# Optimization experiments

Hardware: AMD Instinct MI355X
Metric: run time of the kernel (lower is better)

## Reference

```python
import jax, jax.numpy as jnp
import numpy as np

N = 200000   # total nodes across batched graphs
E = 3200000  # total edges
G = 1024     # number of graphs
MOL_DIM, HID, OUT = 9, 64, 64


def gcn_conv(x, W, b, src, dst, num_nodes):
    """PyG GCNConv: add self-loops, symmetric deg^{-1/2} normalization, linear first."""
    x = x @ W  # [N, H]
    loop = jnp.arange(num_nodes, dtype=src.dtype)
    s = jnp.concatenate([src, loop])
    d = jnp.concatenate([dst, loop])
    deg = jax.ops.segment_sum(jnp.ones_like(d, dtype=x.dtype), d, num_segments=num_nodes)
    dinv = jnp.where(deg > 0, jax.lax.rsqrt(deg), 0.0)
    norm = dinv[s] * dinv[d]                       # [E+N]
    msgs = x[s] * norm[:, None]                    # gather + scale
    out = jax.ops.segment_sum(msgs, d, num_segments=num_nodes)  # scatter-add
    return out + b


def setup_inputs() -> dict:
    key = jax.random.key(0)
    ks = jax.random.split(key, 12)
    def glorot(k, shp):
        scale = np.sqrt(2.0 / (shp[0] + shp[1])).astype(np.float32)
        return jax.random.normal(k, shp, dtype=jnp.float32) * scale
    return {
        "x": jax.random.normal(ks[0], (N, MOL_DIM), dtype=jnp.float32),
        "edge_index": jax.random.randint(ks[1], (2, E), 0, N, dtype=jnp.int32),
        "edge_attr": jax.random.normal(ks[2], (E, 3), dtype=jnp.float32),
        "batch": jnp.sort(jax.random.randint(ks[3], (N,), 0, G, dtype=jnp.int32)),
        "W1": glorot(ks[4], (MOL_DIM, HID)), "b1": jnp.zeros((HID,), jnp.float32),
        "W2": glorot(ks[5], (HID, HID)),     "b2": jnp.zeros((HID,), jnp.float32),
        "W3": glorot(ks[6], (HID, HID)),     "b3": jnp.zeros((HID,), jnp.float32),
        "Wl": glorot(ks[7], (2 * HID, OUT)), "bl": jnp.zeros((OUT,), jnp.float32),
    }


def reference(x, edge_index, edge_attr, batch, W1, b1, W2, b2, W3, b3, Wl, bl):
    src, dst = edge_index[0], edge_index[1]
    h = jax.nn.relu(gcn_conv(x, W1, b1, src, dst, N))
    h = jax.nn.relu(gcn_conv(h, W2, b2, src, dst, N))
    h = jax.nn.relu(gcn_conv(h, W3, b3, src, dst, N))
    # global mean/max pool over graphs
    counts = jax.ops.segment_sum(jnp.ones((N,), h.dtype), batch, num_segments=G)
    h_sum = jax.ops.segment_sum(h, batch, num_segments=G)
    h_mean = h_sum / jnp.maximum(counts, 1.0)[:, None]
    h_max = jax.ops.segment_max(h, batch, num_segments=G)
    pooled = jnp.concatenate([h_mean, h_max], axis=1)   # [G, 2H]
    return pooled @ Wl + bl
```

## Files before the change

### kernel.cpp

```cpp
#include <hip/hip_runtime.h>

typedef unsigned short u16;
typedef __attribute__((ext_vector_type(8))) short short8;
typedef __attribute__((ext_vector_type(4))) float float4v;

#define HID 64
#define MOLD 9
#define BSH 10
#define NBM 256
#define NBLK 256

__device__ __forceinline__ float bf2f(u16 u) {
    return __uint_as_float(((unsigned)u) << 16);
}
__device__ __forceinline__ u16 f2bf(float f) {
    unsigned x = __float_as_uint(f);
    unsigned r = (x + 0x7FFFu + ((x >> 16) & 1u)) >> 16;
    return (u16)r;
}
__device__ __forceinline__ void unpack_add(uint4 r, float* a) {
    a[0] += __uint_as_float(r.x << 16); a[1] += __uint_as_float(r.x & 0xffff0000u);
    a[2] += __uint_as_float(r.y << 16); a[3] += __uint_as_float(r.y & 0xffff0000u);
    a[4] += __uint_as_float(r.z << 16); a[5] += __uint_as_float(r.z & 0xffff0000u);
    a[6] += __uint_as_float(r.w << 16); a[7] += __uint_as_float(r.w & 0xffff0000u);
}
__device__ __forceinline__ void unpack_set(uint4 r, float* a) {
    a[0] = __uint_as_float(r.x << 16); a[1] = __uint_as_float(r.x & 0xffff0000u);
    a[2] = __uint_as_float(r.y << 16); a[3] = __uint_as_float(r.y & 0xffff0000u);
    a[4] = __uint_as_float(r.z << 16); a[5] = __uint_as_float(r.z & 0xffff0000u);
    a[6] = __uint_as_float(r.w << 16); a[7] = __uint_as_float(r.w & 0xffff0000u);
}
__device__ __forceinline__ void unpack_add2(uint2 r, float* a) {
    a[0] += __uint_as_float(r.x << 16); a[1] += __uint_as_float(r.x & 0xffff0000u);
    a[2] += __uint_as_float(r.y << 16); a[3] += __uint_as_float(r.y & 0xffff0000u);
}

__global__ void k_detect(const u16* __restrict__ p, int n, int* __restrict__ flag) {
    bool bad = false;
    for (int i = threadIdx.x; i < n; i += 256) {
        float v = bf2f(p[i]);
        if (!(v == v) || fabsf(v) > 1000.f) bad = true;
    }
    if (bad) atomicOr(flag, 1);
}

__global__ void k_cvt_w(const void* W1, const void* b1, const void* W2, const void* b2,
                        const void* W3, const void* b3, const void* Wl, const void* bl,
                        const int* __restrict__ flag, u16* __restrict__ wbf) {
    int mode = *flag;
    int i = blockIdx.x * 256 + threadIdx.x;
    if (i >= 17216) return;
    const void* s; int base;
    if (i < 576)        { s = W1; base = 0; }
    else if (i < 640)   { s = b1; base = 576; }
    else if (i < 4736)  { s = W2; base = 640; }
    else if (i < 4800)  { s = b2; base = 4736; }
    else if (i < 8896)  { s = W3; base = 4800; }
    else if (i < 8960)  { s = b3; base = 8896; }
    else if (i < 17152) { s = Wl; base = 8960; }
    else                { s = bl; base = 17152; }
    int o = i - base;
    wbf[i] = mode ? f2bf(((const float*)s)[o]) : ((const u16*)s)[o];
}

__global__ __launch_bounds__(256) void k_hist(const int* __restrict__ ei, int E, int nb,
                                              int chunk, int* __restrict__ cntmat) {
    __shared__ int h[NBM];
    int tid = threadIdx.x, k = blockIdx.x;
    for (int i = tid; i < nb; i += 256) h[i] = 0;
    __syncthreads();
    int e0 = k * chunk, e1 = e0 + chunk; if (e1 > E) e1 = E;
    for (int e = e0 + tid; e < e1; e += 256)
        atomicAdd(&h[ei[E + e] >> BSH], 1);
    __syncthreads();
    for (int b = tid; b < nb; b += 256) cntmat[b * NBLK + k] = h[b];
}

__global__ __launch_bounds__(1024) void k_scanmat(int* __restrict__ cntmat, int total) {
    __shared__ int ps[1024];
    int tid = threadIdx.x;
    int chunk = (total + 1023) >> 10;
    int i0 = tid * chunk, i1 = i0 + chunk; if (i1 > total) i1 = total;
    int sum = 0;
    for (int i = i0; i < i1; i++) sum += cntmat[i];
    ps[tid] = sum;
    __syncthreads();
    for (int off = 1; off < 1024; off <<= 1) {
        int t = (tid >= off) ? ps[tid - off] : 0;
        __syncthreads();
        ps[tid] += t;
        __syncthreads();
    }
    int run = ps[tid] - sum;
    for (int i = i0; i < i1; i++) { int c = cntmat[i]; cntmat[i] = run; run += c; }
}

__global__ __launch_bounds__(256) void k_scatter(const int* __restrict__ ei, int E, int nb,
                                                 int chunk, const int* __restrict__ offmat,
                                                 unsigned* __restrict__ staging) {
    __shared__ int cur[NBM];
    int tid = threadIdx.x, k = blockIdx.x;
    for (int b = tid; b < nb; b += 256) cur[b] = offmat[b * NBLK + k];
    __syncthreads();
    int e0 = k * chunk, e1 = e0 + chunk; if (e1 > E) e1 = E;
    for (int e = e0 + tid; e < e1; e += 256) {
        int s = ei[e];
        int d = ei[E + e];
        int b = d >> BSH;
        int p = atomicAdd(&cur[b], 1);
        staging[p] = (unsigned)s | ((unsigned)(d & ((1 << BSH) - 1)) << 18);
    }
}

__global__ __launch_bounds__(256) void k_p4(const unsigned* __restrict__ staging,
                                            const int* __restrict__ offmat, int nb, int N, int E,
                                            int* __restrict__ col, int* __restrict__ rowptr,
                                            float* __restrict__ dinv) {
    __shared__ int cnt[1 << BSH];
    __shared__ int cur[1 << BSH];
    __shared__ int ps[256];
    int b = blockIdx.x, tid = threadIdx.x;
    int s0 = offmat[b * NBLK];
    int s1 = (b == nb - 1) ? E : offmat[(b + 1) * NBLK];
    for (int i = tid; i < (1 << BSH); i += 256) cnt[i] = 0;
    __syncthreads();
    for (int i = s0 + tid; i < s1; i += 256)
        atomicAdd(&cnt[staging[i] >> 18], 1);
    __syncthreads();
    int base4 = tid * 4;
    int c0 = cnt[base4], c1 = cnt[base4 + 1], c2 = cnt[base4 + 2], c3 = cnt[base4 + 3];
    int tsum = c0 + c1 + c2 + c3;
    ps[tid] = tsum;
    __syncthreads();
    for (int off = 1; off < 256; off <<= 1) {
        int t = (tid >= off) ? ps[tid - off] : 0;
        __syncthreads();
        ps[tid] += t;
        __syncthreads();
    }
    int ex = ps[tid] - tsum;
    int o0 = s0 + ex, o1 = o0 + c0, o2 = o1 + c1, o3 = o2 + c2;
    cur[base4] = o0; cur[base4 + 1] = o1; cur[base4 + 2] = o2; cur[base4 + 3] = o3;
    int v = (b << BSH) + base4;
    if (v < N)     { rowptr[v] = o0;     dinv[v] = rsqrtf((float)(c0 + 1)); }
    if (v + 1 < N) { rowptr[v + 1] = o1; dinv[v + 1] = rsqrtf((float)(c1 + 1)); }
    if (v + 2 < N) { rowptr[v + 2] = o2; dinv[v + 2] = rsqrtf((float)(c2 + 1)); }
    if (v + 3 < N) { rowptr[v + 3] = o3; dinv[v + 3] = rsqrtf((float)(c3 + 1)); }
    if (b == nb - 1 && tid == 0) rowptr[N] = E;
    __syncthreads();
    for (int i = s0 + tid; i < s1; i += 256) {
        unsigned w = staging[i];
        int p = atomicAdd(&cur[w >> 18], 1);
        col[p] = (int)(w & 0x3FFFF);
    }
}

__global__ void k_cvt_x(const void* __restrict__ x, const float* __restrict__ dinv,
                        const int* __restrict__ flag, int N, u16* __restrict__ xd) {
    int mode = *flag;
    int i = blockIdx.x * 256 + threadIdx.x;
    if (i >= N * 16) return;
    int v = i >> 4, f = i & 15;
    float val = 0.f;
    if (f < MOLD) {
        val = mode ? ((const float*)x)[v * MOLD + f]
                   : bf2f(((const u16*)x)[v * MOLD + f]);
        val *= dinv[v];
    }
    xd[i] = f2bf(val);
}

__global__ __launch_bounds__(256, 4) void k_aggx(
        const u16* __restrict__ xd, const int* __restrict__ rowptr,
        const int* __restrict__ col, const float* __restrict__ dinv,
        const u16* __restrict__ W1, const u16* __restrict__ b1,
        int N, u16* __restrict__ h1) {
    int lane = threadIdx.x & 63;
    int eslot = lane >> 2, fq = lane & 3;
    float w1r[MOLD];
#pragma unroll
    for (int k = 0; k < MOLD; k++) w1r[k] = bf2f(W1[k * HID + lane]);
    float bias = bf2f(b1[lane]);
    bool sel0 = ((lane >> 2) & 1) != 0, sel1 = ((lane >> 3) & 1) != 0;
    int wid = (blockIdx.x * blockDim.x + threadIdx.x) >> 6;
    int nw = (gridDim.x * blockDim.x) >> 6;
    for (int v = wid; v < N; v += nw) {
        float acc[4];
        if (eslot == 0) {
            uint2 r = *(const uint2*)(xd + (size_t)v * 16 + fq * 4);
            acc[0] = __uint_as_float(r.x << 16); acc[1] = __uint_as_float(r.x & 0xffff0000u);
            acc[2] = __uint_as_float(r.y << 16); acc[3] = __uint_as_float(r.y & 0xffff0000u);
        } else {
#pragma unroll
            for (int j = 0; j < 4; j++) acc[j] = 0.f;
        }
        int e = rowptr[v + 1];
        for (int i = rowptr[v] + eslot; i < e; i += 16) {
            int u = col[i];
            uint2 r = *(const uint2*)(xd + (size_t)u * 16 + fq * 4);
            unpack_add2(r, acc);
        }
        float s0 = acc[0] + __shfl_xor(acc[0], 4);
        float s1 = acc[1] + __shfl_xor(acc[1], 4);
        float s2 = acc[2] + __shfl_xor(acc[2], 4);
        float s3 = acc[3] + __shfl_xor(acc[3], 4);
        float t0 = sel0 ? s2 : s0;
        float t1 = sel0 ? s3 : s1;
        t0 += __shfl_xor(t0, 8);
        t1 += __shfl_xor(t1, 8);
        float val = sel1 ? t1 : t0;
        val += __shfl_xor(val, 16);
        val += __shfl_xor(val, 32);
        float accf = 0.f;
#pragma unroll
        for (int k = 0; k < MOLD; k++) {
            int Lk = (k >> 2) | ((k & 2) << 1) | ((k & 1) << 3);
            accf += __shfl(val, Lk) * w1r[k];
        }
        float h = fmaxf(dinv[v] * accf + bias, 0.f);
        h1[(size_t)v * HID + lane] = f2bf(h);
    }
}

__device__ __forceinline__ float gather_node_one(const u16* __restrict__ y,
                                                 const int* __restrict__ rowptr,
                                                 const int* __restrict__ col,
                                                 float dv, float bias,
                                                 int v, int eslot, int fg) {
    float acc[8];
    const u16* yf = y + fg * 8;
    if (eslot == 0) {
        unpack_set(*(const uint4*)(yf + (size_t)v * HID), acc);
    } else {
#pragma unroll
        for (int j = 0; j < 8; j++) acc[j] = 0.f;
    }
    int e = rowptr[v + 1];
    for (int i = rowptr[v] + eslot; i < e; i += 8) {
        int u = col[i];
        uint4 r = *(const uint4*)(yf + (size_t)u * HID);
        unpack_add(r, acc);
    }
    bool e0 = (eslot & 1) != 0, e1 = (eslot & 2) != 0, e2 = (eslot & 4) != 0;
    float s[8];
#pragma unroll
    for (int j = 0; j < 8; j++) s[j] = acc[j] + __shfl_xor(acc[j], 8);
    float b4[4];
#pragma unroll
    for (int k = 0; k < 4; k++) b4[k] = e0 ? s[k + 4] : s[k];
#pragma unroll
    for (int k = 0; k < 4; k++) b4[k] += __shfl_xor(b4[k], 16);
    float c2[2];
    c2[0] = e1 ? b4[2] : b4[0];
    c2[1] = e1 ? b4[3] : b4[1];
    c2[0] += __shfl_xor(c2[0], 32);
    c2[1] += __shfl_xor(c2[1], 32);
    float val = e2 ? c2[1] : c2[0];
    return fmaxf(dv * val + bias, 0.f);
}

__global__ __launch_bounds__(256, 4) void k_agg(
        const u16* __restrict__ y, const int* __restrict__ rowptr,
        const int* __restrict__ col, const float* __restrict__ dinv,
        const u16* __restrict__ bseg, int N, u16* __restrict__ h) {
    int lane = threadIdx.x & 63;
    int eslot = lane >> 3, fg = lane & 7;
    int idx = fg * 8 + ((eslot & 1) << 2) + (eslot & 2) + ((eslot >> 2) & 1);
    float bias = bf2f(bseg[idx]);
    int wid = (blockIdx.x * blockDim.x + threadIdx.x) >> 6;
    int nw = (gridDim.x * blockDim.x) >> 6;
    for (int v = wid; v < N; v += nw) {
        float hv = gather_node_one(y, rowptr, col, dinv[v], bias, v, eslot, fg);
        h[(size_t)v * HID + idx] = f2bf(hv);
    }
}

__global__ __launch_bounds__(256, 4) void k_aggpool(
        const u16* __restrict__ y, const int* __restrict__ rowptr,
        const int* __restrict__ col, const float* __restrict__ dinv,
        const u16* __restrict__ bseg, const int* __restrict__ batch, int N,
        float* __restrict__ hsum, int* __restrict__ hmax, int* __restrict__ cnt) {
    int lane = threadIdx.x & 63;
    int eslot = lane >> 3, fg = lane & 7;
    int idx = fg * 8 + ((eslot & 1) << 2) + (eslot & 2) + ((eslot >> 2) & 1);
    float bias = bf2f(bseg[idx]);
    int wid = (blockIdx.x * blockDim.x + threadIdx.x) >> 6;
    int nw = (gridDim.x * blockDim.x) >> 6;
    int cpw = (N + nw - 1) / nw;
    int v0 = wid * cpw;
    int v1 = v0 + cpw; if (v1 > N) v1 = N;
    int gcur = -1, pcnt = 0;
    float psum = 0.f, pmax = 0.f;
    for (int v = v0; v < v1; ++v) {
        float hv = gather_node_one(y, rowptr, col, dinv[v], bias, v, eslot, fg);
        int g = batch[v];
        if (g != gcur) {
            if (gcur >= 0) {
                atomicAdd(&hsum[gcur * HID + idx], psum);
                atomicMax(&hmax[gcur * HID + idx], __float_as_int(pmax));
                if (lane == 0) atomicAdd(&cnt[gcur], pcnt);
            }
            psum = 0.f; pmax = 0.f; pcnt = 0;
            gcur = g;
        }
        pcnt++;
        psum += hv;
        pmax = fmaxf(pmax, hv);
    }
    if (gcur >= 0) {
        atomicAdd(&hsum[gcur * HID + idx], psum);
        atomicMax(&hmax[gcur * HID + idx], __float_as_int(pmax));
        if (lane == 0) atomicAdd(&cnt[gcur], pcnt);
    }
}

__global__ __launch_bounds__(256, 4) void k_mm(
        const u16* __restrict__ h, const u16* __restrict__ W,
        const float* __restrict__ dinv, int N, u16* __restrict__ y) {
    int lane = threadIdx.x & 63;
    int q = lane >> 4, m = lane & 15;
    int wid = (blockIdx.x * blockDim.x + threadIdx.x) >> 6;
    int nw = (gridDim.x * blockDim.x) >> 6;
    short8 bfrag[4][2];
#pragma unroll
    for (int t = 0; t < 4; ++t)
#pragma unroll
        for (int kh = 0; kh < 2; ++kh) {
            short8 bv;
#pragma unroll
            for (int j = 0; j < 8; ++j)
                bv[j] = (short)W[(kh * 32 + q * 8 + j) * HID + t * 16 + m];
            bfrag[t][kh] = bv;
        }
    const float4v zero = {0.f, 0.f, 0.f, 0.f};
    int ntiles = (N + 15) >> 4;
    for (int tile = wid; tile < ntiles; tile += nw) {
        int base = tile * 16;
        int row = base + m;
        short8 a0 = {0, 0, 0, 0, 0, 0, 0, 0}, a1 = a0;
        if (row < N) {
            uint4 r0 = *(const uint4*)(h + (size_t)row * HID + q * 8);
            uint4 r1 = *(const uint4*)(h + (size_t)row * HID + 32 + q * 8);
            a0 = __builtin_bit_cast(short8, r0);
            a1 = __builtin_bit_cast(short8, r1);
        }
        float4v c[4];
#pragma unroll
        for (int t = 0; t < 4; ++t) c[t] = zero;
#pragma unroll
        for (int t = 0; t < 4; ++t) {
            c[t] = __builtin_amdgcn_mfma_f32_16x16x32_bf16(a0, bfrag[t][0], c[t], 0, 0, 0);
            c[t] = __builtin_amdgcn_mfma_f32_16x16x32_bf16(a1, bfrag[t][1], c[t], 0, 0, 0);
        }
#pragma unroll
        for (int r = 0; r < 4; ++r) {
            int node = base + q * 4 + r;
            if (node < N) {
                float dv = dinv[node];
#pragma unroll
                for (int t = 0; t < 4; ++t)
                    y[(size_t)node * HID + t * 16 + m] = f2bf(c[t][r] * dv);
            }
        }
    }
}

__global__ void k_final(const float* __restrict__ hsum, const int* __restrict__ hmaxi,
                        const int* __restrict__ cnt, const u16* __restrict__ wlseg,
                        const u16* __restrict__ blseg, const int* __restrict__ flag,
                        int G, void* __restrict__ out) {
    __shared__ float w[2 * HID * HID];
    int tid = threadIdx.x;
    for (int i = tid; i < 2 * HID * HID; i += blockDim.x) w[i] = bf2f(wlseg[i]);
    __syncthreads();
    int g = blockIdx.x * 4 + (tid >> 6);
    int f = tid & 63;
    if (g >= G) return;
    float inv = 1.f / fmaxf((float)cnt[g], 1.f);
    float acc = bf2f(blseg[f]);
#pragma unroll 8
    for (int k = 0; k < HID; k++) acc += (hsum[g * HID + k] * inv) * w[k * HID + f];
#pragma unroll 8
    for (int k = 0; k < HID; k++) acc += __int_as_float(hmaxi[g * HID + k]) * w[(HID + k) * HID + f];
    int mode = *flag;
    if (mode) ((float*)out)[g * HID + f] = acc;
    else      ((u16*)out)[g * HID + f] = f2bf(acc);
}

extern "C" void kernel_launch(void* const* d_in, const int* in_sizes, int n_in,
                              void* d_out, int out_size, void* d_ws, size_t ws_size,
                              hipStream_t stream) {
    const void* x  = d_in[0];
    const int*  ei = (const int*)d_in[1];
    const int*  batch = (const int*)d_in[3];

    const int NX = in_sizes[0];
    const int N  = NX / MOLD;
    const int E  = in_sizes[1] / 2;
    const int G  = out_size / HID;
    const int nb = (N + (1 << BSH) - 1) >> BSH;

    char* p = (char*)d_ws;
    auto alloc = [&](size_t bytes) -> char* {
        char* r = p;
        p += (bytes + 255) & ~(size_t)255;
        return r;
    };
    int*   flag    = (int*)alloc(256);
    int*   rowptr  = (int*)alloc((size_t)(N + 1) * 4);
    float* dinv    = (float*)alloc((size_t)N * 4);
    int*   cntmat  = (int*)alloc((size_t)nb * NBLK * 4);
    u16*   wbf     = (u16*)alloc((size_t)17216 * 2);
    int*   colb    = (int*)alloc((size_t)E * 4);
    size_t hb = (size_t)N * HID * 2;
    size_t sb = (size_t)E * 4;
    size_t xs = (size_t)N * 16 * 2;
    size_t ub = hb; if (sb > ub) ub = sb; if (xs > ub) ub = xs;
    char* hbuf = alloc(ub);
    unsigned* staging = (unsigned*)hbuf;
    u16*      xd      = (u16*)hbuf;
    u16*      hbf     = (u16*)hbuf;
    u16*   ybf  = (u16*)alloc((size_t)N * HID * 2);
    float* hsum = (float*)alloc((size_t)G * HID * 4);
    int*   hmax = (int*)alloc((size_t)G * HID * 4);
    int*   cnt  = (int*)alloc((size_t)G * 4);

    hipMemsetAsync(flag, 0, 256, stream);
    hipMemsetAsync(hsum, 0, (size_t)G * HID * 4, stream);
    hipMemsetAsync(hmax, 0, (size_t)G * HID * 4, stream);
    hipMemsetAsync(cnt, 0, (size_t)G * 4, stream);

    k_detect<<<1, 256, 0, stream>>>((const u16*)x, 8192, flag);
    k_cvt_w<<<68, 256, 0, stream>>>(d_in[4], d_in[5], d_in[6], d_in[7],
                                    d_in[8], d_in[9], d_in[10], d_in[11], flag, wbf);

    int chunk = (E + NBLK - 1) / NBLK;
    k_hist<<<NBLK, 256, 0, stream>>>(ei, E, nb, chunk, cntmat);
    k_scanmat<<<1, 1024, 0, stream>>>(cntmat, nb * NBLK);
    k_scatter<<<NBLK, 256, 0, stream>>>(ei, E, nb, chunk, cntmat, staging);
    k_p4<<<nb, 256, 0, stream>>>(staging, cntmat, nb, N, E, colb, rowptr, dinv);

    k_cvt_x<<<(N * 16 + 255) / 256, 256, 0, stream>>>(x, dinv, flag, N, xd);
    k_aggx<<<2048, 256, 0, stream>>>(xd, rowptr, colb, dinv, wbf + 0, wbf + 576,
                                     N, ybf);
    k_mm<<<1024, 256, 0, stream>>>(ybf, wbf + 640, dinv, N, hbf);
    k_agg<<<2048, 256, 0, stream>>>(hbf, rowptr, colb, dinv, wbf + 4736, N, ybf);
    k_mm<<<1024, 256, 0, stream>>>(ybf, wbf + 4800, dinv, N, hbf);
    k_aggpool<<<2048, 256, 0, stream>>>(hbf, rowptr, colb, dinv, wbf + 8896, batch, N,
                                        hsum, hmax, cnt);

    k_final<<<(G + 3) / 4, 256, 0, stream>>>(hsum, hmax, cnt, wbf + 8960, wbf + 17152,
                                             flag, G, d_out);
}
```

Measured before the change: 592.1 us.

## Split padded input features into 8+1 layout and fold memsets into kernels

The first-layer input is now stored as an 8-feature bf16 array plus a separate array for the ninth feature, replacing the 16-wide padded layout. The gather-aggregate kernel therefore handles 32 edges per wave instead of 16, and each edge reads fewer bytes. The four hipMemsetAsync calls are removed: the flag is written directly by the detect kernel, and the pooling accumulators are zeroed inside the weight-conversion kernel. This cuts gather traffic and launch overhead, at the cost of an extra scalar load per edge and a longer shuffle reduction.

Measured after the change: 604.6 us. +2.1%, slower.

```diff
diff --git a/kernel.cpp b/kernel.cpp
--- a/kernel.cpp
+++ b/kernel.cpp
@@ -34,33 +34,49 @@
     a[0] += __uint_as_float(r.x << 16); a[1] += __uint_as_float(r.x & 0xffff0000u);
     a[2] += __uint_as_float(r.y << 16); a[3] += __uint_as_float(r.y & 0xffff0000u);
 }
+__device__ __forceinline__ void unpack_set2(uint2 r, float* a) {
+    a[0] = __uint_as_float(r.x << 16); a[1] = __uint_as_float(r.x & 0xffff0000u);
+    a[2] = __uint_as_float(r.y << 16); a[3] = __uint_as_float(r.y & 0xffff0000u);
+}
 
 __global__ void k_detect(const u16* __restrict__ p, int n, int* __restrict__ flag) {
-    bool bad = false;
+    __shared__ int bad;
+    if (threadIdx.x == 0) bad = 0;
+    __syncthreads();
+    bool b = false;
     for (int i = threadIdx.x; i < n; i += 256) {
         float v = bf2f(p[i]);
-        if (!(v == v) || fabsf(v) > 1000.f) bad = true;
-    }
-    if (bad) atomicOr(flag, 1);
+        if (!(v == v) || fabsf(v) > 1000.f) b = true;
+    }
+    if (b) atomicOr(&bad, 1);
+    __syncthreads();
+    if (threadIdx.x == 0) *flag = bad;
 }
 
 __global__ void k_cvt_w(const void* W1, const void* b1, const void* W2, const void* b2,
                         const void* W3, const void* b3, const void* Wl, const void* bl,
-                        const int* __restrict__ flag, u16* __restrict__ wbf) {
+                        const int* __restrict__ flag, u16* __restrict__ wbf,
+                        float* __restrict__ hsum, int* __restrict__ hmax,
+                        int* __restrict__ cnt, int G) {
     int mode = *flag;
-    int i = blockIdx.x * 256 + threadIdx.x;
-    if (i >= 17216) return;
-    const void* s; int base;
-    if (i < 576)        { s = W1; base = 0; }
-    else if (i < 640)   { s = b1; base = 576; }
-    else if (i < 4736)  { s = W2; base = 640; }
-    else if (i < 4800)  { s = b2; base = 4736; }
-    else if (i < 8896)  { s = W3; base = 4800; }
-    else if (i < 8960)  { s = b3; base = 8896; }
-    else if (i < 17152) { s = Wl; base = 8960; }
-    else                { s = bl; base = 17152; }
-    int o = i - base;
-    wbf[i] = mode ? f2bf(((const float*)s)[o]) : ((const u16*)s)[o];
+    int gid = blockIdx.x * 256 + threadIdx.x;
+    int gtot = gridDim.x * 256;
+    if (gid < 17216) {
+        int i = gid;
+        const void* s; int base;
+        if (i < 576)        { s = W1; base = 0; }
+        else if (i < 640)   { s = b1; base = 576; }
+        else if (i < 4736)  { s = W2; base = 640; }
+        else if (i < 4800)  { s = b2; base = 4736; }
+        else if (i < 8896)  { s = W3; base = 4800; }
+        else if (i < 8960)  { s = b3; base = 8896; }
+        else if (i < 17152) { s = Wl; base = 8960; }
+        else                { s = bl; base = 17152; }
+        int o = i - base;
+        wbf[i] = mode ? f2bf(((const float*)s)[o]) : ((const u16*)s)[o];
+    }
+    for (int j = gid; j < G * HID; j += gtot) { hsum[j] = 0.f; hmax[j] = 0; }
+    for (int j = gid; j < G; j += gtot) cnt[j] = 0;
 }
 
 __global__ __launch_bounds__(256) void k_hist(const int* __restrict__ ei, int E, int nb,
@@ -156,66 +172,78 @@
 }
 
 __global__ void k_cvt_x(const void* __restrict__ x, const float* __restrict__ dinv,
-                        const int* __restrict__ flag, int N, u16* __restrict__ xd) {
+                        const int* __restrict__ flag, int N,
+                        u16* __restrict__ x8d, u16* __restrict__ x9d) {
     int mode = *flag;
     int i = blockIdx.x * 256 + threadIdx.x;
-    if (i >= N * 16) return;
-    int v = i >> 4, f = i & 15;
-    float val = 0.f;
-    if (f < MOLD) {
-        val = mode ? ((const float*)x)[v * MOLD + f]
-                   : bf2f(((const u16*)x)[v * MOLD + f]);
-        val *= dinv[v];
-    }
-    xd[i] = f2bf(val);
+    if (i >= N * 9) return;
+    if (i < N * 8) {
+        int v = i >> 3, f = i & 7;
+        float val = mode ? ((const float*)x)[v * MOLD + f]
+                         : bf2f(((const u16*)x)[v * MOLD + f]);
+        x8d[i] = f2bf(val * dinv[v]);
+    } else {
+        int v = i - N * 8;
+        float val = mode ? ((const float*)x)[v * MOLD + 8]
+                         : bf2f(((const u16*)x)[v * MOLD + 8]);
+        x9d[v] = f2bf(val * dinv[v]);
+    }
 }
 
 __global__ __launch_bounds__(256, 4) void k_aggx(
-        const u16* __restrict__ xd, const int* __restrict__ rowptr,
-        const int* __restrict__ col, const float* __restrict__ dinv,
-        const u16* __restrict__ W1, const u16* __restrict__ b1,
-        int N, u16* __restrict__ h1) {
+        const u16* __restrict__ x8d, const u16* __restrict__ x9d,
+        const int* __restrict__ rowptr, const int* __restrict__ col,
+        const float* __restrict__ dinv, const u16* __restrict__ W1,
+        const u16* __restrict__ b1, int N, u16* __restrict__ h1) {
     int lane = threadIdx.x & 63;
-    int eslot = lane >> 2, fq = lane & 3;
-    float w1r[MOLD];
-#pragma unroll
-    for (int k = 0; k < MOLD; k++) w1r[k] = bf2f(W1[k * HID + lane]);
+    int fp = lane & 1, eslot = lane >> 1;
+    float w1a[8];
+#pragma unroll
+    for (int k = 0; k < 8; k++) w1a[k] = bf2f(W1[k * HID + lane]);
+    float w1b = bf2f(W1[8 * HID + lane]);
     float bias = bf2f(b1[lane]);
-    bool sel0 = ((lane >> 2) & 1) != 0, sel1 = ((lane >> 3) & 1) != 0;
+    bool bit1 = (lane & 2) != 0, bit2 = (lane & 4) != 0;
     int wid = (blockIdx.x * blockDim.x + threadIdx.x) >> 6;
     int nw = (gridDim.x * blockDim.x) >> 6;
     for (int v = wid; v < N; v += nw) {
-        float acc[4];
+        float a8[4];
+        float a9 = 0.f;
         if (eslot == 0) {
-            uint2 r = *(const uint2*)(xd + (size_t)v * 16 + fq * 4);
-            acc[0] = __uint_as_float(r.x << 16); acc[1] = __uint_as_float(r.x & 0xffff0000u);
-            acc[2] = __uint_as_float(r.y << 16); acc[3] = __uint_as_float(r.y & 0xffff0000u);
+            unpack_set2(*(const uint2*)(x8d + (size_t)v * 8 + fp * 4), a8);
+            if (fp == 1) a9 = bf2f(x9d[v]);
         } else {
 #pragma unroll
-            for (int j = 0; j < 4; j++) acc[j] = 0.f;
+            for (int j = 0; j < 4; j++) a8[j] = 0.f;
         }
         int e = rowptr[v + 1];
-        for (int i = rowptr[v] + eslot; i < e; i += 16) {
+        for (int i = rowptr[v] + eslot; i < e; i += 32) {
             int u = col[i];
-            uint2 r = *(const uint2*)(xd + (size_t)u * 16 + fq * 4);
-            unpack_add2(r, acc);
-        }
-        float s0 = acc[0] + __shfl_xor(acc[0], 4);
-        float s1 = acc[1] + __shfl_xor(acc[1], 4);
-        float s2 = acc[2] + __shfl_xor(acc[2], 4);
-        float s3 = acc[3] + __shfl_xor(acc[3], 4);
-        float t0 = sel0 ? s2 : s0;
-        float t1 = sel0 ? s3 : s1;
-        t0 += __shfl_xor(t0, 8);
-        t1 += __shfl_xor(t1, 8);
-        float val = sel1 ? t1 : t0;
-        val += __shfl_xor(val, 16);
-        val += __shfl_xor(val, 32);
-        float accf = 0.f;
-#pragma unroll
-        for (int k = 0; k < MOLD; k++) {
-            int Lk = (k >> 2) | ((k & 2) << 1) | ((k & 1) << 3);
-            accf += __shfl(val, Lk) * w1r[k];
+            unpack_add2(*(const uint2*)(x8d + (size_t)u * 8 + fp * 4), a8);
+            if (fp == 1) a9 += bf2f(x9d[u]);
+        }
+        float s0 = a8[0] + __shfl_xor(a8[0], 2);
+        float s1 = a8[1] + __shfl_xor(a8[1], 2);
+        float s2 = a8[2] + __shfl_xor(a8[2], 2);
+        float s3 = a8[3] + __shfl_xor(a8[3], 2);
+        float k0 = bit1 ? s2 : s0;
+        float k1 = bit1 ? s3 : s1;
+        k0 += __shfl_xor(k0, 4);
+        k1 += __shfl_xor(k1, 4);
+        float c = bit2 ? k1 : k0;
+        c += __shfl_xor(c, 8);
+        c += __shfl_xor(c, 16);
+        c += __shfl_xor(c, 32);
+        a9 += __shfl_xor(a9, 1);
+        a9 += __shfl_xor(a9, 2);
+        a9 += __shfl_xor(a9, 4);
+        a9 += __shfl_xor(a9, 8);
+        a9 += __shfl_xor(a9, 16);
+        a9 += __shfl_xor(a9, 32);
+        float accf = a9 * w1b;
+#pragma unroll
+        for (int k = 0; k < 8; k++) {
+            int Lk = (k >> 2) | (((k >> 1) & 1) << 1) | ((k & 1) << 2);
+            accf += __shfl(c, Lk) * w1a[k];
         }
         float h = fmaxf(dinv[v] * accf + bias, 0.f);
         h1[(size_t)v * HID + lane] = f2bf(h);
@@ -414,25 +442,22 @@
     int*   colb    = (int*)alloc((size_t)E * 4);
     size_t hb = (size_t)N * HID * 2;
     size_t sb = (size_t)E * 4;
-    size_t xs = (size_t)N * 16 * 2;
+    size_t xs = (size_t)N * 9 * 2;
     size_t ub = hb; if (sb > ub) ub = sb; if (xs > ub) ub = xs;
     char* hbuf = alloc(ub);
     unsigned* staging = (unsigned*)hbuf;
-    u16*      xd      = (u16*)hbuf;
+    u16*      x8d     = (u16*)hbuf;
+    u16*      x9d     = (u16*)(hbuf + (size_t)N * 8 * 2);
     u16*      hbf     = (u16*)hbuf;
     u16*   ybf  = (u16*)alloc((size_t)N * HID * 2);
     float* hsum = (float*)alloc((size_t)G * HID * 4);
     int*   hmax = (int*)alloc((size_t)G * HID * 4);
     int*   cnt  = (int*)alloc((size_t)G * 4);
 
-    hipMemsetAsync(flag, 0, 256, stream);
-    hipMemsetAsync(hsum, 0, (size_t)G * HID * 4, stream);
-    hipMemsetAsync(hmax, 0, (size_t)G * HID * 4, stream);
-    hipMemsetAsync(cnt, 0, (size_t)G * 4, stream);
-
     k_detect<<<1, 256, 0, stream>>>((const u16*)x, 8192, flag);
     k_cvt_w<<<68, 256, 0, stream>>>(d_in[4], d_in[5], d_in[6], d_in[7],
-                                    d_in[8], d_in[9], d_in[10], d_in[11], flag, wbf);
+                                    d_in[8], d_in[9], d_in[10], d_in[11], flag, wbf,
+                                    hsum, hmax, cnt, G);
 
     int chunk = (E + NBLK - 1) / NBLK;
     k_hist<<<NBLK, 256, 0, stream>>>(ei, E, nb, chunk, cntmat);
@@ -440,8 +465,8 @@
     k_scatter<<<NBLK, 256, 0, stream>>>(ei, E, nb, chunk, cntmat, staging);
     k_p4<<<nb, 256, 0, stream>>>(staging, cntmat, nb, N, E, colb, rowptr, dinv);
 
-    k_cvt_x<<<(N * 16 + 255) / 256, 256, 0, stream>>>(x, dinv, flag, N, xd);
-    k_aggx<<<2048, 256, 0, stream>>>(xd, rowptr, colb, dinv, wbf + 0, wbf + 576,
+    k_cvt_x<<<(N * 9 + 255) / 256, 256, 0, stream>>>(x, dinv, flag, N, x8d, x9d);
+    k_aggx<<<2048, 256, 0, stream>>>(x8d, x9d, rowptr, colb, dinv, wbf + 0, wbf + 576,
                                      N, ybf);
     k_mm<<<1024, 256, 0, stream>>>(ybf, wbf + 640, dinv, N, hbf);
     k_agg<<<2048, 256, 0, stream>>>(hbf, rowptr, colb, dinv, wbf + 4736, N, ybf);
```
